# Performance work log

Hardware: AMD Instinct MI355X
Metric: run time of the kernel (lower is better)

## Reference

```python
import jax, jax.numpy as jnp
import numpy as np

# MORRConfig_20um_MQ (all-pass MRR) constants used by mrr_roundtrip_phase_to_tr(intensity=True)
A = 0.987   # attenuation_factor a
R = 0.99    # coupling_factor r
KS, STRIDE, PAD = 3, 1, 1
IN_C, OUT_C, MB = 32, 64, 8


def _unfold(x, ks, pad, stride):
    # torch.nn.functional.unfold: output channel order is (C, kh, kw), C slowest
    B, C, H, W = x.shape
    xp = jnp.pad(x, ((0, 0), (0, 0), (pad, pad), (pad, pad)))
    Ho = (H + 2 * pad - ks) // stride + 1
    Wo = (W + 2 * pad - ks) // stride + 1
    cols = jnp.stack(
        [xp[:, :, i:i + stride * Ho:stride, j:j + stride * Wo:stride]
         for i in range(ks) for j in range(ks)],
        axis=2,
    )  # [B, C, ks*ks, Ho, Wo]
    return cols.reshape(B, C * ks * ks, Ho * Wo), Ho, Wo


def _mrr_tr(phase):
    # all-pass MRR intensity transmission vs roundtrip phase detuning
    c = jnp.cos(phase)
    return (A * A - 2.0 * A * R * c + R * R) / (1.0 - 2.0 * A * R * c + (A * R) ** 2)


def setup_inputs() -> dict:
    key = jax.random.key(0)
    k1, k2, k3 = jax.random.split(key, 3)
    B, H, W = 8, 64, 64
    wic = IN_C * KS * KS           # 288, divisible by miniblock -> no zero pad
    q = wic // MB                  # grid_dim_x = 36
    p = OUT_C // MB                # grid_dim_y = 8
    x = jax.random.normal(k1, (B, IN_C, H, W), jnp.float32)
    weight = jax.random.normal(k2, (p, q, MB), jnp.float32)
    morr_output_scale = jax.random.normal(k3, (max(1, q // 2) + 1,), jnp.float32)
    return {"x": x, "weight": weight, "morr_output_scale": morr_output_scale}


def reference(x, weight, morr_output_scale):
    B = x.shape[0]
    p, q, k = weight.shape
    w = jnp.abs(weight)                                  # w_bit=16 -> build_weight() = |W|
    cols, Ho, Wo = _unfold(x, KS, PAD, STRIDE)           # [B, wic, L]
    xf = cols.transpose(0, 2, 1).reshape(-1, q, k)       # [N, q, k], N = B*Ho*Wo
    xf = xf * xf                                         # intensity modulation x^2
    # block-circulant matvec via rFFT (circular convolution per (p, q) block)
    Xf = jnp.fft.rfft(xf, n=k, axis=-1)                  # [N, q, kf]
    Wf = jnp.fft.rfft(w, n=k, axis=-1)                   # [p, q, kf]
    phase = jnp.fft.irfft(Xf[:, None, :, :] * Wf[None, :, :, :], n=k, axis=-1)  # [N, p, q, k]
    tr = _mrr_tr(phase)                                  # MORR nonlinear transfer
    # differential-rail output scale (even grid_dim_x branch)
    s = morr_output_scale
    if q % 2 == 0:
        scale = jnp.concatenate([s[:-1], -s[:-1]])
    else:
        scale = jnp.concatenate([s[:-1], s[-1:], -s[:-1]])
    out = jnp.einsum('npqk,q->npk', tr, scale).reshape(-1, p * k)[:, :OUT_C]
    return out.reshape(B, Ho, Wo, OUT_C).transpose(0, 3, 1, 2)  # [B, OUT_C, Ho, Wo]
```

## Files before the change

### kernel.cpp

```cpp
#include <hip/hip_runtime.h>
#include <hip/hip_fp16.h>
#include <math.h>
#include <utility>


typedef _Float16 f16x8 __attribute__((ext_vector_type(8)));
typedef float    f32x4 __attribute__((ext_vector_type(4)));
typedef unsigned int u32;
typedef u32 u32x4 __attribute__((ext_vector_type(4)));

template <class F, size_t... I>
__device__ __forceinline__ void sf_impl(F&& f, std::index_sequence<I...>) {
    (f(std::integral_constant<size_t, I>{}), ...);
}
template <size_t N, class F>
__device__ __forceinline__ void static_for(F&& f) {
    sf_impl(f, std::make_index_sequence<N>{});
}

__device__ __forceinline__ u32 pck(float a, float b) {
    _Float16 ha = (_Float16)a, hb = (_Float16)b;
    return (u32)__builtin_bit_cast(unsigned short, ha) |
           ((u32)__builtin_bit_cast(unsigned short, hb) << 16);
}

#define INV2PI 0.15915494309189535f

__global__ void bprep(const float* __restrict__ wg, u32* __restrict__ bt) {
    int tid = blockIdx.x * 256 + threadIdx.x;
    int nthr = gridDim.x * 256;
    for (int e = tid; e < 288 * 68; e += nthr) {
        int slot = e / 68, wi = e - slot * 68;
        u32 val = 0u;
        if (wi < 64) {
            int hl = slot & 1, qpt = slot >> 1;
            int q = qpt >> 2, pt = qpt & 3;
            int l = wi >> 2, jp = wi & 3;
            int flat = pt * 16 + l, p = flat >> 3, t = flat & 7;
            float wa = fabsf(wg[(p * 36 + q) * 8 + ((t - 2 * jp) & 7)]) * INV2PI;
            float wb = fabsf(wg[(p * 36 + q) * 8 + ((t - 2 * jp - 1) & 7)]) * INV2PI;
            _Float16 ha = (_Float16)wa, hb = (_Float16)wb;
            if (hl == 0) {
                val = pck((float)ha, (float)hb);
            } else {
                val = pck(wa - (float)ha, wb - (float)hb);
            }
        }
        bt[e] = val;
    }
}

__global__ __launch_bounds__(256, 4)
void morr_mfma(const float* __restrict__ xg, const u32* __restrict__ bt,
               const float* __restrict__ sg, float* __restrict__ out) {
    __shared__ union {
        u32   x[3200];
        float o[64 * 65];
    } sm;

    constexpr double Ad = 0.987, Rd = 0.99;
    constexpr float K2  = (float)(2.0 * Ad * Rd);
    constexpr float C2  = (float)(1.0 + (Ad * Rd) * (Ad * Rd));
    constexpr float NDK = (float)(-(1.0 - Ad * Ad) * (1.0 - Rd * Rd) * (2.0 * Ad * Rd));

    const int tid = threadIdx.x;
    const int b   = blockIdx.z;
    const int gr0 = blockIdx.y * 8, gc0 = blockIdx.x * 8;

    for (int i = tid; i < 3200; i += 256) {
        int c = i / 100, rem = i - c * 100;
        int r = rem / 10, cl = rem - r * 10;
        int gr = gr0 - 1 + r, gc = gc0 - 1 + cl;
        float v = 0.f;
        if ((unsigned)gr < 64u && (unsigned)gc < 64u)
            v = xg[((b * 32 + c) * 64 + gr) * 64 + gc];
        v = v * v;
        _Float16 h = (_Float16)v;
        sm.x[i] = pck((float)h, v - (float)h);
    }
    __syncthreads();

    const int lane = tid & 63;
    const int wv   = tid >> 6;
    const int c16  = lane & 15;
    const int pix  = wv * 16 + c16;
    const int abase = (pix >> 3) * 10 + (pix & 7);
    const int lnw  = (lane < 16) ? (lane << 2) : 64;

    float oacc[4][4];
    static_for<4>([&](auto P) { static_for<4>([&](auto R) { oacc[P][R] = 0.f; }); });

    #pragma unroll 1
    for (int qp = 0; qp < 18; ++qp) {
        const int q0 = qp, q1 = qp + 18;
        u32 xw0[8], xw1[8];
        static_for<8>([&](auto J) {
            constexpr int j = J;
            const int ci0 = q0 * 8 + j, c0 = ci0 / 9, rm0 = ci0 - c0 * 9;
            const int ci1 = q1 * 8 + j, c1 = ci1 / 9, rm1 = ci1 - c1 * 9;
            xw0[j] = sm.x[abase + c0 * 100 + (rm0 / 3) * 10 + (rm0 - (rm0 / 3) * 3)];
            xw1[j] = sm.x[abase + c1 * 100 + (rm1 / 3) * 10 + (rm1 - (rm1 / 3) * 3)];
        });
        u32x4 a0h, a0l, a1h, a1l;
        static_for<4>([&](auto JP) {
            constexpr int jp = JP;
            a0h[jp] = (xw0[2 * jp] & 0xFFFFu) | (xw0[2 * jp + 1] << 16);
            a0l[jp] = (xw0[2 * jp] >> 16) | (xw0[2 * jp + 1] & 0xFFFF0000u);
            a1h[jp] = (xw1[2 * jp] & 0xFFFFu) | (xw1[2 * jp + 1] << 16);
            a1l[jp] = (xw1[2 * jp] >> 16) | (xw1[2 * jp + 1] & 0xFFFF0000u);
        });
        const f16x8 A0h = __builtin_bit_cast(f16x8, a0h);
        const f16x8 A0l = __builtin_bit_cast(f16x8, a0l);
        const f16x8 A1h = __builtin_bit_cast(f16x8, a1h);
        const f16x8 A1l = __builtin_bit_cast(f16x8, a1l);

        f32x4 ph0[4], ph1[4];
        static_for<4>([&](auto PT) {
            constexpr int pt = PT;
            const u32x4 b0h = *reinterpret_cast<const u32x4*>(bt + ((q0 * 4 + pt) * 2 + 0) * 68 + lnw);
            const u32x4 b0l = *reinterpret_cast<const u32x4*>(bt + ((q0 * 4 + pt) * 2 + 1) * 68 + lnw);
            const u32x4 b1h = *reinterpret_cast<const u32x4*>(bt + ((q1 * 4 + pt) * 2 + 0) * 68 + lnw);
            const u32x4 b1l = *reinterpret_cast<const u32x4*>(bt + ((q1 * 4 + pt) * 2 + 1) * 68 + lnw);
            f32x4 z = {0.f, 0.f, 0.f, 0.f};
            f32x4 acc0 = __builtin_amdgcn_mfma_f32_16x16x32_f16(A0l, __builtin_bit_cast(f16x8, b0h), z, 0, 0, 0);
            acc0 = __builtin_amdgcn_mfma_f32_16x16x32_f16(A0h, __builtin_bit_cast(f16x8, b0l), acc0, 0, 0, 0);
            acc0 = __builtin_amdgcn_mfma_f32_16x16x32_f16(A0h, __builtin_bit_cast(f16x8, b0h), acc0, 0, 0, 0);
            f32x4 acc1 = __builtin_amdgcn_mfma_f32_16x16x32_f16(A1l, __builtin_bit_cast(f16x8, b1h), z, 0, 0, 0);
            acc1 = __builtin_amdgcn_mfma_f32_16x16x32_f16(A1h, __builtin_bit_cast(f16x8, b1l), acc1, 0, 0, 0);
            acc1 = __builtin_amdgcn_mfma_f32_16x16x32_f16(A1h, __builtin_bit_cast(f16x8, b1h), acc1, 0, 0, 0);
            ph0[pt] = acc0;
            ph1[pt] = acc1;
        });

        const float sv = sg[qp];
        static_for<4>([&](auto PT) {
            constexpr int pt = PT;
            static_for<4>([&](auto R) {
                constexpr int r = R;
                float cA = __builtin_amdgcn_cosf(ph0[pt][r]);
                float cB = __builtin_amdgcn_cosf(ph1[pt][r]);
                float da = fmaf(-K2, cA, C2);
                float db = fmaf(-K2, cB, C2);
                float rr = __builtin_amdgcn_rcpf(da * db);
                oacc[pt][r] = fmaf(sv, (cA - cB) * rr, oacc[pt][r]);
            });
        });
    }

    __syncthreads();
    static_for<4>([&](auto PT) {
        constexpr int pt = PT;
        static_for<4>([&](auto R) {
            constexpr int r = R;
            const int oc  = pt * 16 + c16;
            const int pxr = wv * 16 + (lane >> 4) * 4 + r;
            sm.o[oc * 65 + pxr] = NDK * oacc[pt][r];
        });
    });
    __syncthreads();
    for (int i = 0; i < 16; ++i) {
        int flat = i * 256 + tid;
        int oc = flat >> 6, px = flat & 63;
        out[((b * 64 + oc) * 64 + gr0 + (px >> 3)) * 64 + gc0 + (px & 7)] = sm.o[oc * 65 + px];
    }
}

extern "C" void kernel_launch(void* const* d_in, const int* in_sizes, int n_in,
                              void* d_out, int out_size, void* d_ws, size_t ws_size,
                              hipStream_t stream) {
    const float* x = (const float*)d_in[0];
    const float* w = (const float*)d_in[1];
    const float* s = (const float*)d_in[2];
    float* outp = (float*)d_out;
    u32* bt = (u32*)d_ws;
    hipLaunchKernelGGL(bprep, dim3(32), dim3(256), 0, stream, w, bt);
    dim3 grid(8, 8, 8);
    hipLaunchKernelGGL(morr_mfma, grid, dim3(256), 0, stream, x, bt, s, outp);
}
```

Measured before the change: 103.1 us.

## Split output-channel groups across blocks to raise parallelism and occupancy

Each block now handles one of four 16-channel output groups instead of all 64, so the grid grows from 8x8x8 to 32x8x8 and per-thread accumulators shrink from 16 to 4. Launch bounds move to 8 waves per SIMD and the output staging buffer shrinks. Smaller blocks and more of them should help with latency hiding and occupancy. The cost is that each block reloads and squares its input halo tile, so that staging work is repeated four times.

```diff
diff --git a/kernel.cpp b/kernel.cpp
--- a/kernel.cpp
+++ b/kernel.cpp
@@ -40,22 +40,19 @@
             float wa = fabsf(wg[(p * 36 + q) * 8 + ((t - 2 * jp) & 7)]) * INV2PI;
             float wb = fabsf(wg[(p * 36 + q) * 8 + ((t - 2 * jp - 1) & 7)]) * INV2PI;
             _Float16 ha = (_Float16)wa, hb = (_Float16)wb;
-            if (hl == 0) {
-                val = pck((float)ha, (float)hb);
-            } else {
-                val = pck(wa - (float)ha, wb - (float)hb);
-            }
+            if (hl == 0) val = pck((float)ha, (float)hb);
+            else         val = pck(wa - (float)ha, wb - (float)hb);
         }
         bt[e] = val;
     }
 }
 
-__global__ __launch_bounds__(256, 4)
+__global__ __launch_bounds__(256, 8)
 void morr_mfma(const float* __restrict__ xg, const u32* __restrict__ bt,
                const float* __restrict__ sg, float* __restrict__ out) {
     __shared__ union {
         u32   x[3200];
-        float o[64 * 65];
+        float o[16 * 68];
     } sm;
 
     constexpr double Ad = 0.987, Rd = 0.99;
@@ -65,7 +62,9 @@
 
     const int tid = threadIdx.x;
     const int b   = blockIdx.z;
-    const int gr0 = blockIdx.y * 8, gc0 = blockIdx.x * 8;
+    const int ptg = blockIdx.x & 3;
+    const int gc0 = (blockIdx.x >> 2) * 8;
+    const int gr0 = blockIdx.y * 8;
 
     for (int i = tid; i < 3200; i += 256) {
         int c = i / 100, rem = i - c * 100;
@@ -87,8 +86,8 @@
     const int abase = (pix >> 3) * 10 + (pix & 7);
     const int lnw  = (lane < 16) ? (lane << 2) : 64;
 
-    float oacc[4][4];
-    static_for<4>([&](auto P) { static_for<4>([&](auto R) { oacc[P][R] = 0.f; }); });
+    float oacc[4];
+    static_for<4>([&](auto R) { oacc[R] = 0.f; });
 
     #pragma unroll 1
     for (int qp = 0; qp < 18; ++qp) {
@@ -114,55 +113,44 @@
         const f16x8 A1h = __builtin_bit_cast(f16x8, a1h);
         const f16x8 A1l = __builtin_bit_cast(f16x8, a1l);
 
-        f32x4 ph0[4], ph1[4];
-        static_for<4>([&](auto PT) {
-            constexpr int pt = PT;
-            const u32x4 b0h = *reinterpret_cast<const u32x4*>(bt + ((q0 * 4 + pt) * 2 + 0) * 68 + lnw);
-            const u32x4 b0l = *reinterpret_cast<const u32x4*>(bt + ((q0 * 4 + pt) * 2 + 1) * 68 + lnw);
-            const u32x4 b1h = *reinterpret_cast<const u32x4*>(bt + ((q1 * 4 + pt) * 2 + 0) * 68 + lnw);
-            const u32x4 b1l = *reinterpret_cast<const u32x4*>(bt + ((q1 * 4 + pt) * 2 + 1) * 68 + lnw);
-            f32x4 z = {0.f, 0.f, 0.f, 0.f};
-            f32x4 acc0 = __builtin_amdgcn_mfma_f32_16x16x32_f16(A0l, __builtin_bit_cast(f16x8, b0h), z, 0, 0, 0);
-            acc0 = __builtin_amdgcn_mfma_f32_16x16x32_f16(A0h, __builtin_bit_cast(f16x8, b0l), acc0, 0, 0, 0);
-            acc0 = __builtin_amdgcn_mfma_f32_16x16x32_f16(A0h, __builtin_bit_cast(f16x8, b0h), acc0, 0, 0, 0);
-            f32x4 acc1 = __builtin_amdgcn_mfma_f32_16x16x32_f16(A1l, __builtin_bit_cast(f16x8, b1h), z, 0, 0, 0);
-            acc1 = __builtin_amdgcn_mfma_f32_16x16x32_f16(A1h, __builtin_bit_cast(f16x8, b1l), acc1, 0, 0, 0);
-            acc1 = __builtin_amdgcn_mfma_f32_16x16x32_f16(A1h, __builtin_bit_cast(f16x8, b1h), acc1, 0, 0, 0);
-            ph0[pt] = acc0;
-            ph1[pt] = acc1;
-        });
+        const u32x4 b0h = *reinterpret_cast<const u32x4*>(bt + ((q0 * 4 + ptg) * 2 + 0) * 68 + lnw);
+        const u32x4 b0l = *reinterpret_cast<const u32x4*>(bt + ((q0 * 4 + ptg) * 2 + 1) * 68 + lnw);
+        const u32x4 b1h = *reinterpret_cast<const u32x4*>(bt + ((q1 * 4 + ptg) * 2 + 0) * 68 + lnw);
+        const u32x4 b1l = *reinterpret_cast<const u32x4*>(bt + ((q1 * 4 + ptg) * 2 + 1) * 68 + lnw);
+        f32x4 z = {0.f, 0.f, 0.f, 0.f};
+        f32x4 ph0 = __builtin_amdgcn_mfma_f32_16x16x32_f16(A0l, __builtin_bit_cast(f16x8, b0h), z, 0, 0, 0);
+        ph0 = __builtin_amdgcn_mfma_f32_16x16x32_f16(A0h, __builtin_bit_cast(f16x8, b0l), ph0, 0, 0, 0);
+        ph0 = __builtin_amdgcn_mfma_f32_16x16x32_f16(A0h, __builtin_bit_cast(f16x8, b0h), ph0, 0, 0, 0);
+        f32x4 ph1 = __builtin_amdgcn_mfma_f32_16x16x32_f16(A1l, __builtin_bit_cast(f16x8, b1h), z, 0, 0, 0);
+        ph1 = __builtin_amdgcn_mfma_f32_16x16x32_f16(A1h, __builtin_bit_cast(f16x8, b1l), ph1, 0, 0, 0);
+        ph1 = __builtin_amdgcn_mfma_f32_16x16x32_f16(A1h, __builtin_bit_cast(f16x8, b1h), ph1, 0, 0, 0);
 
         const float sv = sg[qp];
-        static_for<4>([&](auto PT) {
-            constexpr int pt = PT;
-            static_for<4>([&](auto R) {
-                constexpr int r = R;
-                float cA = __builtin_amdgcn_cosf(ph0[pt][r]);
-                float cB = __builtin_amdgcn_cosf(ph1[pt][r]);
-                float da = fmaf(-K2, cA, C2);
-                float db = fmaf(-K2, cB, C2);
-                float rr = __builtin_amdgcn_rcpf(da * db);
-                oacc[pt][r] = fmaf(sv, (cA - cB) * rr, oacc[pt][r]);
-            });
+        static_for<4>([&](auto R) {
+            constexpr int r = R;
+            float cA = __builtin_amdgcn_cosf(ph0[r]);
+            float cB = __builtin_amdgcn_cosf(ph1[r]);
+            float da = fmaf(-K2, cA, C2);
+            float db = fmaf(-K2, cB, C2);
+            float rr = __builtin_amdgcn_rcpf(da * db);
+            oacc[r] = fmaf(sv, (cA - cB) * rr, oacc[r]);
         });
     }
 
     __syncthreads();
-    static_for<4>([&](auto PT) {
-        constexpr int pt = PT;
-        static_for<4>([&](auto R) {
-            constexpr int r = R;
-            const int oc  = pt * 16 + c16;
-            const int pxr = wv * 16 + (lane >> 4) * 4 + r;
-            sm.o[oc * 65 + pxr] = NDK * oacc[pt][r];
-        });
+    static_for<4>([&](auto R) {
+        constexpr int r = R;
+        const int pxr = wv * 16 + (lane >> 4) * 4 + r;
+        sm.o[c16 * 68 + pxr] = NDK * oacc[r];
     });
     __syncthreads();
-    for (int i = 0; i < 16; ++i) {
-        int flat = i * 256 + tid;
-        int oc = flat >> 6, px = flat & 63;
-        out[((b * 64 + oc) * 64 + gr0 + (px >> 3)) * 64 + gc0 + (px & 7)] = sm.o[oc * 65 + px];
-    }
+    static_for<4>([&](auto I) {
+        constexpr int i = I;
+        const int flat = i * 256 + tid;
+        const int ocl = flat >> 6, px = flat & 63;
+        out[((b * 64 + ptg * 16 + ocl) * 64 + gr0 + (px >> 3)) * 64 + gc0 + (px & 7)]
+            = sm.o[ocl * 68 + px];
+    });
 }
 
 extern "C" void kernel_launch(void* const* d_in, const int* in_sizes, int n_in,
@@ -174,6 +162,6 @@
     float* outp = (float*)d_out;
     u32* bt = (u32*)d_ws;
     hipLaunchKernelGGL(bprep, dim3(32), dim3(256), 0, stream, w, bt);
-    dim3 grid(8, 8, 8);
+    dim3 grid(32, 8, 8);
     hipLaunchKernelGGL(morr_mfma, grid, dim3(256), 0, stream, x, bt, s, outp);
 }
```

New measurement: 136.8 us. +32.7%, slower.
